# Kernel tuning notes

Measured on AMD Instinct MI355X. Metric: run time of the kernel, lower is better.

The kernel has to match this reference:

```python
import jax, jax.numpy as jnp
from jax import lax
import numpy as np

T, D, H, E, K = 4096, 1024, 2048, 8, 2

def setup_inputs() -> dict:
    key = jax.random.key(0)
    ks = jax.random.split(key, 5)
    x = jax.random.normal(ks[0], (T, D), dtype=jnp.float32)
    weights = jax.random.uniform(ks[1], (T, K), dtype=jnp.float32)
    indices = jax.random.randint(ks[2], (T, K), 0, E, dtype=jnp.int64)
    # GatedMLP params (bias=False): fc1 weight [2H, D], fc2 weight [D, H], stacked over experts
    W1 = jax.random.normal(ks[3], (E, 2 * H, D), dtype=jnp.float32) * 0.02
    W2 = jax.random.normal(ks[4], (E, D, H), dtype=jnp.float32) * 0.02
    return {"x": x, "weights": weights, "indices": indices, "W1": W1, "W2": W2}

def reference(x, weights, indices, W1, W2):
    # Combine per-token routing weights into a per-(token, expert) weight matrix.
    # Tokens not routed to expert e get weight 0, so the dense per-expert GatedMLP
    # weighted-sum is mathematically identical to the gather->MLP->scatter-add loop.
    onehot = jax.nn.one_hot(indices, E, dtype=weights.dtype)        # [T, K, E]
    w_te = jnp.einsum('tke,tk->et', onehot, weights)                # [E, T]

    def body(y, carry):
        W1e, W2e, we = carry                                        # [2H,D], [D,H], [T]
        h = x @ W1e.T                                               # [T, 2H]
        u, gate = jnp.split(h, 2, axis=-1)                          # [T, H] each
        out = (u * jax.nn.silu(gate)) @ W2e.T                       # [T, D]
        return y + out * we[:, None], None

    y, _ = lax.scan(body, jnp.zeros_like(x), (W1, W2, w_te))
    return y
```

## Files before the change

### kernel.cpp

```cpp
#include <hip/hip_runtime.h>
#include <stdint.h>

#define T_TOK 4096
#define D_DIM 1024
#define H_DIM 2048
#define E_EXP 8
#define K_TOP 2
#define NTK   (T_TOK * K_TOP)
#define MTILE 192
#define MAX_TILES 56

typedef short bf16x8 __attribute__((ext_vector_type(8)));
typedef float f32x4  __attribute__((ext_vector_type(4)));

#define MINI(a, b) ((a) < (b) ? (a) : (b))

__device__ __forceinline__ unsigned short f2bf(float f) {
  unsigned u = __float_as_uint(f);
  u += 0x7fffu + ((u >> 16) & 1u);
  return (unsigned short)(u >> 16);
}

#define GLDS16(gp, lp)                                                        \
  __builtin_amdgcn_global_load_lds(                                           \
      (const __attribute__((address_space(1))) void*)(gp),                    \
      (__attribute__((address_space(3))) void*)(lp), 16, 0, 0)



__global__ __launch_bounds__(256) void k_route_count(const int* __restrict__ idx,
                                                     int* __restrict__ meta) {
  __shared__ int h[E_EXP];
  int tid = threadIdx.x;
  if (tid < E_EXP) h[tid] = 0;
  __syncthreads();
  int i = blockIdx.x * 256 + tid;
  atomicAdd(&h[idx[i] & (E_EXP - 1)], 1);
  __syncthreads();
  if (tid < E_EXP) atomicAdd(&meta[tid], h[tid]);
}

__global__ __launch_bounds__(64) void k_route_plan(int* __restrict__ meta) {
  if (threadIdx.x) return;
  int off = 0, nt = 0;
  for (int e = 0; e < E_EXP; ++e) {
    int c = meta[e];
    meta[8 + e]  = off;
    meta[16 + e] = off;
    for (int r = 0; r < c; r += MTILE) {
      meta[32 + nt]  = e;
      meta[112 + nt] = off + r;
      meta[192 + nt] = MINI(MTILE, c - r);
      ++nt;
    }
    off += c;
  }
  meta[24] = nt;
}

__global__ __launch_bounds__(256) void k_route_scatter(const int* __restrict__ idx,
                                                       const float* __restrict__ w,
                                                       int* __restrict__ meta,
                                                       int* __restrict__ rows,
                                                       float* __restrict__ wv) {
  __shared__ int h[E_EXP], base[E_EXP];
  int tid = threadIdx.x;
  if (tid < E_EXP) h[tid] = 0;
  __syncthreads();
  int i = blockIdx.x * 256 + tid;
  int e = idx[i] & (E_EXP - 1);
  int r = atomicAdd(&h[e], 1);
  __syncthreads();
  if (tid < E_EXP) base[tid] = atomicAdd(&meta[16 + tid], h[tid]);
  __syncthreads();
  int p = base[e] + r;
  rows[p] = i >> 1;
  wv[p]   = w[i];
}

#define NX8   (T_TOK * D_DIM / 8)
#define NW18  (E_EXP * 2 * H_DIM * D_DIM / 8)
#define NW28  (E_EXP * D_DIM * H_DIM / 8)
#define NCVT8 (NX8 + NW18 + NW28)

__global__ __launch_bounds__(256) void k_cvt8(const float* __restrict__ x,
                                              const float* __restrict__ W1,
                                              const float* __restrict__ W2,
                                              unsigned short* __restrict__ xb,
                                              unsigned short* __restrict__ W1b,
                                              unsigned short* __restrict__ W2b) {
  long gid = (long)blockIdx.x * 256 + threadIdx.x;
  const float* src;
  unsigned short* dst;
  long i;
  if (gid < NX8) {
    src = x; dst = xb; i = gid;
  } else if (gid < NX8 + NW18) {
    src = W1; dst = W1b; i = gid - NX8;
  } else if (gid < NCVT8) {
    src = W2; dst = W2b; i = gid - (NX8 + NW18);
  } else return;
  float4 a = ((const float4*)src)[2 * i];
  float4 b = ((const float4*)src)[2 * i + 1];
  uint4 o;
  o.x = f2bf(a.x) | ((unsigned)f2bf(a.y) << 16);
  o.y = f2bf(a.z) | ((unsigned)f2bf(a.w) << 16);
  o.z = f2bf(b.x) | ((unsigned)f2bf(b.y) << 16);
  o.w = f2bf(b.z) | ((unsigned)f2bf(b.w) << 16);
  ((uint4*)dst)[i] = o;
}

__global__ __launch_bounds__(512, 2) void k_gemm1(
    const unsigned short* __restrict__ xb,
    const unsigned short* __restrict__ W1b,
    const int* __restrict__ meta,
    const int* __restrict__ rows,
    const float* __restrict__ wv,
    unsigned short* __restrict__ act) {
  int nt = meta[24];
  int tb = blockIdx.x;
  if (tb >= nt) return;
  int e     = meta[32 + tb];
  int r0    = meta[112 + tb];
  int valid = meta[192 + tb];
  int n0    = blockIdx.y * 128;

  __shared__ unsigned short lA[2][MTILE * 64];
  __shared__ unsigned short lB1[2][128 * 64];
  __shared__ unsigned short lB2[2][128 * 64];

  int tid  = threadIdx.x;
  int wave = tid >> 6, lane = tid & 63;
  int wm = wave >> 2, wn = wave & 3;

  const unsigned short* w1e = W1b + (size_t)e * (4096 * 1024);

  const unsigned short *pA[3], *pB1[2], *pB2[2];
#pragma unroll
  for (int it = 0; it < 3; ++it) {
    int c = it * 512 + tid;
    int r = c >> 3, cc = c & 7;
    int g = cc ^ (r & 7);
    int tok = rows[r0 + MINI(r, valid - 1)];
    pA[it] = xb + (size_t)tok * 1024 + g * 8;
  }
#pragma unroll
  for (int it = 0; it < 2; ++it) {
    int c = it * 512 + tid;
    int r = c >> 3, cc = c & 7;
    int g = cc ^ (r & 7);
    pB1[it] = w1e + (size_t)(n0 + r) * 1024 + g * 8;
    pB2[it] = w1e + (size_t)(2048 + n0 + r) * 1024 + g * 8;
  }

  auto STAGE = [&](int t, int b) {
    int k0 = t * 64;
#pragma unroll
    for (int it = 0; it < 3; ++it)
      GLDS16(pA[it] + k0, &lA[b][(it * 512 + wave * 64) * 8]);
#pragma unroll
    for (int it = 0; it < 2; ++it) {
      int lb = (it * 512 + wave * 64) * 8;
      GLDS16(pB1[it] + k0, &lB1[b][lb]);
      GLDS16(pB2[it] + k0, &lB2[b][lb]);
    }
  };

  f32x4 zero = {0.f, 0.f, 0.f, 0.f};
  f32x4 au[6][2], ag[6][2];
#pragma unroll
  for (int i = 0; i < 6; ++i)
#pragma unroll
    for (int j = 0; j < 2; ++j) { au[i][j] = zero; ag[i][j] = zero; }

  int fr = lane & 15, q = lane >> 4;

  STAGE(0, 0);
  for (int t = 0; t < 16; ++t) {
    int cb = t & 1;
    if (t < 15) {
      STAGE(t + 1, cb ^ 1);
      asm volatile("s_waitcnt vmcnt(7)" ::: "memory");
    } else {
      asm volatile("s_waitcnt vmcnt(0)" ::: "memory");
    }
    __builtin_amdgcn_s_barrier();
    __builtin_amdgcn_sched_barrier(0);
#pragma unroll
    for (int kk = 0; kk < 2; ++kk) {
      int co = (((kk << 2) + q) ^ (fr & 7)) * 8 + fr * 64;
      bf16x8 a[6];
#pragma unroll
      for (int i = 0; i < 6; ++i)
        a[i] = *(const bf16x8*)&lA[cb][(wm * 96 + i * 16) * 64 + co];
#pragma unroll
      for (int j = 0; j < 2; ++j) {
        bf16x8 bu = *(const bf16x8*)&lB1[cb][(wn * 32 + j * 16) * 64 + co];
        bf16x8 bg = *(const bf16x8*)&lB2[cb][(wn * 32 + j * 16) * 64 + co];
#pragma unroll
        for (int i = 0; i < 6; ++i) {
          au[i][j] = __builtin_amdgcn_mfma_f32_16x16x32_bf16(a[i], bu, au[i][j], 0, 0, 0);
          ag[i][j] = __builtin_amdgcn_mfma_f32_16x16x32_bf16(a[i], bg, ag[i][j], 0, 0, 0);
        }
      }
    }
    __builtin_amdgcn_s_barrier();
    __builtin_amdgcn_sched_barrier(0);
  }

#pragma unroll
  for (int i = 0; i < 6; ++i) {
#pragma unroll
    for (int reg = 0; reg < 4; ++reg) {
      int lm = wm * 96 + i * 16 + q * 4 + reg;
      if (lm < valid) {
        float wrow = wv[r0 + lm];
        size_t orow = (size_t)(r0 + lm) * 2048;
#pragma unroll
        for (int j = 0; j < 2; ++j) {
          float u = au[i][j][reg];
          float g = ag[i][j][reg];
          float s = g / (1.f + __expf(-g));
          act[orow + (n0 + wn * 32 + j * 16 + fr)] = f2bf(u * s * wrow);
        }
      }
    }
  }
}

__global__ __launch_bounds__(256, 2) void k_gemm2(
    const unsigned short* __restrict__ act,
    const unsigned short* __restrict__ W2b,
    const int* __restrict__ meta,
    const int* __restrict__ rows,
    float* __restrict__ out) {
  int nt = meta[24];
  int tb = blockIdx.x;
  if (tb >= nt) return;
  int e     = meta[32 + tb];
  int r0    = meta[112 + tb];
  int valid = meta[192 + tb];
  int n0    = blockIdx.y * 128;

  __shared__ unsigned short lA[2][MTILE * 64];
  __shared__ unsigned short lB[2][128 * 64];

  int tid  = threadIdx.x;
  int wave = tid >> 6, lane = tid & 63;
  int wm = wave >> 1, wn = wave & 1;

  const unsigned short* w2e = W2b + (size_t)e * (1024 * 2048);

  const unsigned short *pA[6], *pB[4];
#pragma unroll
  for (int it = 0; it < 6; ++it) {
    int c = it * 256 + tid;
    int r = c >> 3, cc = c & 7;
    int g = cc ^ (r & 7);
    pA[it] = act + (size_t)(r0 + MINI(r, valid - 1)) * 2048 + g * 8;
  }
#pragma unroll
  for (int it = 0; it < 4; ++it) {
    int c = it * 256 + tid;
    int r = c >> 3, cc = c & 7;
    int g = cc ^ (r & 7);
    pB[it] = w2e + (size_t)(n0 + r) * 2048 + g * 8;
  }

  auto STAGE = [&](int t, int b) {
    int k0 = t * 64;
#pragma unroll
    for (int it = 0; it < 6; ++it)
      GLDS16(pA[it] + k0, &lA[b][(it * 256 + wave * 64) * 8]);
#pragma unroll
    for (int it = 0; it < 4; ++it)
      GLDS16(pB[it] + k0, &lB[b][(it * 256 + wave * 64) * 8]);
  };

  f32x4 zero = {0.f, 0.f, 0.f, 0.f};
  f32x4 acc[6][4];
#pragma unroll
  for (int i = 0; i < 6; ++i)
#pragma unroll
    for (int j = 0; j < 4; ++j) acc[i][j] = zero;

  int fr = lane & 15, q = lane >> 4;

  STAGE(0, 0);
  for (int t = 0; t < 32; ++t) {
    int cb = t & 1;
    if (t < 31) {
      STAGE(t + 1, cb ^ 1);
      asm volatile("s_waitcnt vmcnt(10)" ::: "memory");
    } else {
      asm volatile("s_waitcnt vmcnt(0)" ::: "memory");
    }
    __builtin_amdgcn_s_barrier();
    __builtin_amdgcn_sched_barrier(0);
#pragma unroll
    for (int kk = 0; kk < 2; ++kk) {
      int co = (((kk << 2) + q) ^ (fr & 7)) * 8 + fr * 64;
      bf16x8 a[6];
#pragma unroll
      for (int i = 0; i < 6; ++i)
        a[i] = *(const bf16x8*)&lA[cb][(wm * 96 + i * 16) * 64 + co];
#pragma unroll
      for (int j = 0; j < 4; ++j) {
        bf16x8 b = *(const bf16x8*)&lB[cb][(wn * 64 + j * 16) * 64 + co];
#pragma unroll
        for (int i = 0; i < 6; ++i)
          acc[i][j] = __builtin_amdgcn_mfma_f32_16x16x32_bf16(a[i], b, acc[i][j], 0, 0, 0);
      }
    }
    __builtin_amdgcn_s_barrier();
    __builtin_amdgcn_sched_barrier(0);
  }

#pragma unroll
  for (int i = 0; i < 6; ++i) {
#pragma unroll
    for (int reg = 0; reg < 4; ++reg) {
      int lm = wm * 96 + i * 16 + q * 4 + reg;
      if (lm < valid) {
        int tok = rows[r0 + lm];
        float* op = out + (size_t)tok * 1024;
#pragma unroll
        for (int j = 0; j < 4; ++j)
          atomicAdd(&op[n0 + wn * 64 + j * 16 + fr], acc[i][j][reg]);
      }
    }
  }
}

extern "C" void kernel_launch(void* const* d_in, const int* in_sizes, int n_in,
                              void* d_out, int out_size, void* d_ws, size_t ws_size,
                              hipStream_t stream) {
  const float* x  = (const float*)d_in[0];
  const float* w  = (const float*)d_in[1];
  const int*  idx = (const int*)d_in[2];
  const float* W1 = (const float*)d_in[3];
  const float* W2 = (const float*)d_in[4];
  float* out = (float*)d_out;

  char* ws = (char*)d_ws;
  unsigned short* W1b = (unsigned short*)(ws);
  unsigned short* W2b = (unsigned short*)(ws + 67108864);
  unsigned short* xb  = (unsigned short*)(ws + 100663296);
  unsigned short* act = (unsigned short*)(ws + 109051904);
  int*   rows = (int*)(ws + 142606336);
  float* wv   = (float*)(ws + 142639104);
  int*   meta = (int*)(ws + 142671872);

  hipMemsetAsync(d_out, 0, (size_t)out_size * sizeof(float), stream);
  hipMemsetAsync(meta, 0, 1088, stream);

  k_cvt8<<<(NCVT8 + 255) / 256, 256, 0, stream>>>(x, W1, W2, xb, W1b, W2b);
  k_route_count<<<32, 256, 0, stream>>>(idx, meta);
  k_route_plan<<<1, 64, 0, stream>>>(meta);
  k_route_scatter<<<32, 256, 0, stream>>>(idx, w, meta, rows, wv);

  dim3 g1(MAX_TILES, H_DIM / 128);
  dim3 g2(MAX_TILES, D_DIM / 128);
  k_gemm1<<<g1, 512, 0, stream>>>(xb, W1b, meta, rows, wv, act);
  k_gemm2<<<g2, 256, 0, stream>>>(act, W2b, meta, rows, out);
}
```

Before: 462.1 us.

## Restructure MoE GEMMs with separate tile sizes, 4-stage pipeline, and XCD-aware block mapping

Both grouped GEMM kernels are rewritten. gemm1 now uses 256-row tiles and gemm2 uses 128-row tiles, with a separate routing plan for each. The loads become a 4-slot ring buffer with K-step 32, loads for future stages issue between two MFMA half-phases under setprio, and the LDS swizzle is new. A 1-D grid remaps block IDs so that blocks sharing an expert tile land on the same XCD, aiming for better L2 reuse and deeper latency hiding. This adds more barriers per step and finer-grained waits, and the wave mapping changes occupancy.

After: 495.1 us. 1.07x slower.

```diff
diff --git a/kernel.cpp b/kernel.cpp
--- a/kernel.cpp
+++ b/kernel.cpp
@@ -7,13 +7,16 @@
 #define E_EXP 8
 #define K_TOP 2
 #define NTK   (T_TOK * K_TOP)
-#define MTILE 192
-#define MAX_TILES 56
+#define MT1 256
+#define MT2 128
+#define MAXT1 48
+#define MAXT2 72
 
 typedef short bf16x8 __attribute__((ext_vector_type(8)));
 typedef float f32x4  __attribute__((ext_vector_type(4)));
 
 #define MINI(a, b) ((a) < (b) ? (a) : (b))
+#define MFMA_BF16 __builtin_amdgcn_mfma_f32_16x16x32_bf16
 
 __device__ __forceinline__ unsigned short f2bf(float f) {
   unsigned u = __float_as_uint(f);
@@ -25,7 +28,6 @@
   __builtin_amdgcn_global_load_lds(                                           \
       (const __attribute__((address_space(1))) void*)(gp),                    \
       (__attribute__((address_space(3))) void*)(lp), 16, 0, 0)
-
 
 
 __global__ __launch_bounds__(256) void k_route_count(const int* __restrict__ idx,
@@ -42,20 +44,27 @@
 
 __global__ __launch_bounds__(64) void k_route_plan(int* __restrict__ meta) {
   if (threadIdx.x) return;
-  int off = 0, nt = 0;
+  int off = 0, nt1 = 0, nt2 = 0;
   for (int e = 0; e < E_EXP; ++e) {
     int c = meta[e];
     meta[8 + e]  = off;
     meta[16 + e] = off;
-    for (int r = 0; r < c; r += MTILE) {
-      meta[32 + nt]  = e;
-      meta[112 + nt] = off + r;
-      meta[192 + nt] = MINI(MTILE, c - r);
-      ++nt;
+    for (int r = 0; r < c; r += MT1) {
+      meta[32 + nt1]  = e;
+      meta[80 + nt1]  = off + r;
+      meta[128 + nt1] = MINI(MT1, c - r);
+      ++nt1;
+    }
+    for (int r = 0; r < c; r += MT2) {
+      meta[176 + nt2] = e;
+      meta[248 + nt2] = off + r;
+      meta[320 + nt2] = MINI(MT2, c - r);
+      ++nt2;
     }
     off += c;
   }
-  meta[24] = nt;
+  meta[24] = nt1;
+  meta[25] = nt2;
 }
 
 __global__ __launch_bounds__(256) void k_route_scatter(const int* __restrict__ idx,
@@ -117,111 +126,156 @@
     const int* __restrict__ rows,
     const float* __restrict__ wv,
     unsigned short* __restrict__ act) {
+  int bid = blockIdx.x;
   int nt = meta[24];
-  int tb = blockIdx.x;
+  int xcd = bid & 7, jj = bid >> 3;
+  int y   = jj & 15;
+  int tb  = ((jj >> 4) << 3) + xcd;
   if (tb >= nt) return;
   int e     = meta[32 + tb];
-  int r0    = meta[112 + tb];
-  int valid = meta[192 + tb];
-  int n0    = blockIdx.y * 128;
-
-  __shared__ unsigned short lA[2][MTILE * 64];
-  __shared__ unsigned short lB1[2][128 * 64];
-  __shared__ unsigned short lB2[2][128 * 64];
+  int r0    = meta[80 + tb];
+  int valid = meta[128 + tb];
+  int n0    = y << 7;
+
+  __shared__ unsigned short lA[4][8192];
+  __shared__ unsigned short lB[4][8192];
 
   int tid  = threadIdx.x;
   int wave = tid >> 6, lane = tid & 63;
   int wm = wave >> 2, wn = wave & 3;
+  int fr = lane & 15, q = lane >> 4;
+  int swz8 = (q ^ ((fr >> 1) & 3)) << 3;
 
   const unsigned short* w1e = W1b + (size_t)e * (4096 * 1024);
 
-  const unsigned short *pA[3], *pB1[2], *pB2[2];
-#pragma unroll
-  for (int it = 0; it < 3; ++it) {
-    int c = it * 512 + tid;
-    int r = c >> 3, cc = c & 7;
-    int g = cc ^ (r & 7);
+  const unsigned short *pA[2], *pB[2];
+#pragma unroll
+  for (int it = 0; it < 2; ++it) {
+    int s = it * 512 + tid;
+    int r = s >> 2;
+    int c = (s & 3) ^ ((s >> 3) & 3);
     int tok = rows[r0 + MINI(r, valid - 1)];
-    pA[it] = xb + (size_t)tok * 1024 + g * 8;
-  }
-#pragma unroll
-  for (int it = 0; it < 2; ++it) {
-    int c = it * 512 + tid;
-    int r = c >> 3, cc = c & 7;
-    int g = cc ^ (r & 7);
-    pB1[it] = w1e + (size_t)(n0 + r) * 1024 + g * 8;
-    pB2[it] = w1e + (size_t)(2048 + n0 + r) * 1024 + g * 8;
-  }
-
-  auto STAGE = [&](int t, int b) {
-    int k0 = t * 64;
-#pragma unroll
-    for (int it = 0; it < 3; ++it)
-      GLDS16(pA[it] + k0, &lA[b][(it * 512 + wave * 64) * 8]);
-#pragma unroll
-    for (int it = 0; it < 2; ++it) {
-      int lb = (it * 512 + wave * 64) * 8;
-      GLDS16(pB1[it] + k0, &lB1[b][lb]);
-      GLDS16(pB2[it] + k0, &lB2[b][lb]);
-    }
+    pA[it] = xb + (size_t)tok * 1024 + c * 8;
+    int wrow = (r < 128) ? (n0 + r) : (1920 + n0 + r);
+    pB[it] = w1e + (size_t)wrow * 1024 + c * 8;
+  }
+
+  auto ISSUE_A = [&](int g) {
+    int sl = g & 3, ko = g * 32;
+#pragma unroll
+    for (int it = 0; it < 2; ++it)
+      GLDS16(pA[it] + ko, &lA[sl][(it * 512 + wave * 64) * 8]);
   };
+  auto ISSUE_B = [&](int g) {
+    int sl = g & 3, ko = g * 32;
+#pragma unroll
+    for (int it = 0; it < 2; ++it)
+      GLDS16(pB[it] + ko, &lB[sl][(it * 512 + wave * 64) * 8]);
+  };
 
   f32x4 zero = {0.f, 0.f, 0.f, 0.f};
-  f32x4 au[6][2], ag[6][2];
-#pragma unroll
-  for (int i = 0; i < 6; ++i)
-#pragma unroll
-    for (int j = 0; j < 2; ++j) { au[i][j] = zero; ag[i][j] = zero; }
-
-  int fr = lane & 15, q = lane >> 4;
-
-  STAGE(0, 0);
-  for (int t = 0; t < 16; ++t) {
-    int cb = t & 1;
-    if (t < 15) {
-      STAGE(t + 1, cb ^ 1);
-      asm volatile("s_waitcnt vmcnt(7)" ::: "memory");
-    } else {
-      asm volatile("s_waitcnt vmcnt(0)" ::: "memory");
-    }
-    __builtin_amdgcn_s_barrier();
-    __builtin_amdgcn_sched_barrier(0);
-#pragma unroll
-    for (int kk = 0; kk < 2; ++kk) {
-      int co = (((kk << 2) + q) ^ (fr & 7)) * 8 + fr * 64;
-      bf16x8 a[6];
-#pragma unroll
-      for (int i = 0; i < 6; ++i)
-        a[i] = *(const bf16x8*)&lA[cb][(wm * 96 + i * 16) * 64 + co];
-#pragma unroll
-      for (int j = 0; j < 2; ++j) {
-        bf16x8 bu = *(const bf16x8*)&lB1[cb][(wn * 32 + j * 16) * 64 + co];
-        bf16x8 bg = *(const bf16x8*)&lB2[cb][(wn * 32 + j * 16) * 64 + co];
-#pragma unroll
-        for (int i = 0; i < 6; ++i) {
-          au[i][j] = __builtin_amdgcn_mfma_f32_16x16x32_bf16(a[i], bu, au[i][j], 0, 0, 0);
-          ag[i][j] = __builtin_amdgcn_mfma_f32_16x16x32_bf16(a[i], bg, ag[i][j], 0, 0, 0);
-        }
-      }
-    }
-    __builtin_amdgcn_s_barrier();
-    __builtin_amdgcn_sched_barrier(0);
-  }
-
-#pragma unroll
-  for (int i = 0; i < 6; ++i) {
+  f32x4 au[8][2], ag[8][2];
+#pragma unroll
+  for (int i = 0; i < 8; ++i)
+#pragma unroll
+    for (int n = 0; n < 2; ++n) { au[i][n] = zero; ag[i][n] = zero; }
+
+  int abase = ((wm << 7) + fr) * 32 + swz8;
+  int ubase = ((wn << 5) + fr) * 32 + swz8;
+
+  ISSUE_A(0); ISSUE_B(0);
+  ISSUE_A(1); ISSUE_B(1);
+  ISSUE_A(2); ISSUE_B(2);
+  asm volatile("s_waitcnt vmcnt(8)" ::: "memory");
+  __builtin_amdgcn_s_barrier();
+
+  for (int g = 0; g < 32; ++g) {
+    int sl = g & 3;
+    const unsigned short* A = lA[sl];
+    const unsigned short* B = lB[sl];
+
+    bf16x8 a0 = *(const bf16x8*)&A[abase + 0 * 512];
+    bf16x8 a1 = *(const bf16x8*)&A[abase + 1 * 512];
+    bf16x8 a2 = *(const bf16x8*)&A[abase + 2 * 512];
+    bf16x8 a3 = *(const bf16x8*)&A[abase + 3 * 512];
+    bf16x8 bu0 = *(const bf16x8*)&B[ubase];
+    bf16x8 bu1 = *(const bf16x8*)&B[ubase + 512];
+    bf16x8 bg0 = *(const bf16x8*)&B[ubase + 4096];
+    bf16x8 bg1 = *(const bf16x8*)&B[ubase + 4608];
+    if (g < 29) ISSUE_A(g + 3);
+    __builtin_amdgcn_sched_barrier(0);
+    __builtin_amdgcn_s_barrier();
+    asm volatile("s_waitcnt lgkmcnt(0)" ::: "memory");
+    __builtin_amdgcn_sched_barrier(0);
+    __builtin_amdgcn_s_setprio(1);
+    au[0][0] = MFMA_BF16(a0, bu0, au[0][0], 0, 0, 0);
+    au[0][1] = MFMA_BF16(a0, bu1, au[0][1], 0, 0, 0);
+    ag[0][0] = MFMA_BF16(a0, bg0, ag[0][0], 0, 0, 0);
+    ag[0][1] = MFMA_BF16(a0, bg1, ag[0][1], 0, 0, 0);
+    au[1][0] = MFMA_BF16(a1, bu0, au[1][0], 0, 0, 0);
+    au[1][1] = MFMA_BF16(a1, bu1, au[1][1], 0, 0, 0);
+    ag[1][0] = MFMA_BF16(a1, bg0, ag[1][0], 0, 0, 0);
+    ag[1][1] = MFMA_BF16(a1, bg1, ag[1][1], 0, 0, 0);
+    au[2][0] = MFMA_BF16(a2, bu0, au[2][0], 0, 0, 0);
+    au[2][1] = MFMA_BF16(a2, bu1, au[2][1], 0, 0, 0);
+    ag[2][0] = MFMA_BF16(a2, bg0, ag[2][0], 0, 0, 0);
+    ag[2][1] = MFMA_BF16(a2, bg1, ag[2][1], 0, 0, 0);
+    au[3][0] = MFMA_BF16(a3, bu0, au[3][0], 0, 0, 0);
+    au[3][1] = MFMA_BF16(a3, bu1, au[3][1], 0, 0, 0);
+    ag[3][0] = MFMA_BF16(a3, bg0, ag[3][0], 0, 0, 0);
+    ag[3][1] = MFMA_BF16(a3, bg1, ag[3][1], 0, 0, 0);
+    __builtin_amdgcn_s_setprio(0);
+    __builtin_amdgcn_sched_barrier(0);
+    __builtin_amdgcn_s_barrier();
+
+    bf16x8 a4 = *(const bf16x8*)&A[abase + 2048 + 0 * 512];
+    bf16x8 a5 = *(const bf16x8*)&A[abase + 2048 + 1 * 512];
+    bf16x8 a6 = *(const bf16x8*)&A[abase + 2048 + 2 * 512];
+    bf16x8 a7 = *(const bf16x8*)&A[abase + 2048 + 3 * 512];
+    if (g < 29) ISSUE_B(g + 3);
+    if (g < 29)      asm volatile("s_waitcnt vmcnt(8)" ::: "memory");
+    else if (g == 29) asm volatile("s_waitcnt vmcnt(4)" ::: "memory");
+    else if (g == 30) asm volatile("s_waitcnt vmcnt(0)" ::: "memory");
+    __builtin_amdgcn_sched_barrier(0);
+    __builtin_amdgcn_s_barrier();
+    asm volatile("s_waitcnt lgkmcnt(0)" ::: "memory");
+    __builtin_amdgcn_sched_barrier(0);
+    __builtin_amdgcn_s_setprio(1);
+    au[4][0] = MFMA_BF16(a4, bu0, au[4][0], 0, 0, 0);
+    au[4][1] = MFMA_BF16(a4, bu1, au[4][1], 0, 0, 0);
+    ag[4][0] = MFMA_BF16(a4, bg0, ag[4][0], 0, 0, 0);
+    ag[4][1] = MFMA_BF16(a4, bg1, ag[4][1], 0, 0, 0);
+    au[5][0] = MFMA_BF16(a5, bu0, au[5][0], 0, 0, 0);
+    au[5][1] = MFMA_BF16(a5, bu1, au[5][1], 0, 0, 0);
+    ag[5][0] = MFMA_BF16(a5, bg0, ag[5][0], 0, 0, 0);
+    ag[5][1] = MFMA_BF16(a5, bg1, ag[5][1], 0, 0, 0);
+    au[6][0] = MFMA_BF16(a6, bu0, au[6][0], 0, 0, 0);
+    au[6][1] = MFMA_BF16(a6, bu1, au[6][1], 0, 0, 0);
+    ag[6][0] = MFMA_BF16(a6, bg0, ag[6][0], 0, 0, 0);
+    ag[6][1] = MFMA_BF16(a6, bg1, ag[6][1], 0, 0, 0);
+    au[7][0] = MFMA_BF16(a7, bu0, au[7][0], 0, 0, 0);
+    au[7][1] = MFMA_BF16(a7, bu1, au[7][1], 0, 0, 0);
+    ag[7][0] = MFMA_BF16(a7, bg0, ag[7][0], 0, 0, 0);
+    ag[7][1] = MFMA_BF16(a7, bg1, ag[7][1], 0, 0, 0);
+    __builtin_amdgcn_s_setprio(0);
+    __builtin_amdgcn_sched_barrier(0);
+    __builtin_amdgcn_s_barrier();
+  }
+
+#pragma unroll
+  for (int mi = 0; mi < 8; ++mi) {
 #pragma unroll
     for (int reg = 0; reg < 4; ++reg) {
-      int lm = wm * 96 + i * 16 + q * 4 + reg;
+      int lm = (wm << 7) + mi * 16 + q * 4 + reg;
       if (lm < valid) {
         float wrow = wv[r0 + lm];
-        size_t orow = (size_t)(r0 + lm) * 2048;
-#pragma unroll
-        for (int j = 0; j < 2; ++j) {
-          float u = au[i][j][reg];
-          float g = ag[i][j][reg];
-          float s = g / (1.f + __expf(-g));
-          act[orow + (n0 + wn * 32 + j * 16 + fr)] = f2bf(u * s * wrow);
+        size_t orow = (size_t)(r0 + lm) * 2048 + n0 + (wn << 5);
+#pragma unroll
+        for (int n = 0; n < 2; ++n) {
+          float u = au[mi][n][reg];
+          float gg = ag[mi][n][reg];
+          float s = gg / (1.f + __expf(-gg));
+          act[orow + n * 16 + fr] = f2bf(u * s * wrow);
         }
       }
     }
@@ -234,99 +288,121 @@
     const int* __restrict__ meta,
     const int* __restrict__ rows,
     float* __restrict__ out) {
-  int nt = meta[24];
-  int tb = blockIdx.x;
+  int bid = blockIdx.x;
+  int nt = meta[25];
+  int xcd = bid & 7, jj = bid >> 3;
+  int y   = jj & 7;
+  int tb  = ((jj >> 3) << 3) + xcd;
   if (tb >= nt) return;
-  int e     = meta[32 + tb];
-  int r0    = meta[112 + tb];
-  int valid = meta[192 + tb];
-  int n0    = blockIdx.y * 128;
-
-  __shared__ unsigned short lA[2][MTILE * 64];
-  __shared__ unsigned short lB[2][128 * 64];
+  int e     = meta[176 + tb];
+  int r0    = meta[248 + tb];
+  int valid = meta[320 + tb];
+  int n0    = y << 7;
+
+  __shared__ unsigned short lA[4][4096];
+  __shared__ unsigned short lB[4][4096];
 
   int tid  = threadIdx.x;
   int wave = tid >> 6, lane = tid & 63;
   int wm = wave >> 1, wn = wave & 1;
+  int fr = lane & 15, q = lane >> 4;
+  int swz8 = (q ^ ((fr >> 1) & 3)) << 3;
 
   const unsigned short* w2e = W2b + (size_t)e * (1024 * 2048);
 
-  const unsigned short *pA[6], *pB[4];
-#pragma unroll
-  for (int it = 0; it < 6; ++it) {
-    int c = it * 256 + tid;
-    int r = c >> 3, cc = c & 7;
-    int g = cc ^ (r & 7);
-    pA[it] = act + (size_t)(r0 + MINI(r, valid - 1)) * 2048 + g * 8;
-  }
-#pragma unroll
-  for (int it = 0; it < 4; ++it) {
-    int c = it * 256 + tid;
-    int r = c >> 3, cc = c & 7;
-    int g = cc ^ (r & 7);
-    pB[it] = w2e + (size_t)(n0 + r) * 2048 + g * 8;
-  }
-
-  auto STAGE = [&](int t, int b) {
-    int k0 = t * 64;
-#pragma unroll
-    for (int it = 0; it < 6; ++it)
-      GLDS16(pA[it] + k0, &lA[b][(it * 256 + wave * 64) * 8]);
-#pragma unroll
-    for (int it = 0; it < 4; ++it)
-      GLDS16(pB[it] + k0, &lB[b][(it * 256 + wave * 64) * 8]);
+  const unsigned short *pA[2], *pB[2];
+#pragma unroll
+  for (int it = 0; it < 2; ++it) {
+    int s = it * 256 + tid;
+    int r = s >> 2;
+    int c = (s & 3) ^ ((s >> 3) & 3);
+    pA[it] = act + (size_t)(r0 + MINI(r, valid - 1)) * 2048 + c * 8;
+    pB[it] = w2e + (size_t)(n0 + r) * 2048 + c * 8;
+  }
+
+  auto ISSUE_A = [&](int g) {
+    int sl = g & 3, ko = g * 32;
+#pragma unroll
+    for (int it = 0; it < 2; ++it)
+      GLDS16(pA[it] + ko, &lA[sl][(it * 256 + wave * 64) * 8]);
   };
+  auto ISSUE_B = [&](int g) {
+    int sl = g & 3, ko = g * 32;
+#pragma unroll
+    for (int it = 0; it < 2; ++it)
+      GLDS16(pB[it] + ko, &lB[sl][(it * 256 + wave * 64) * 8]);
+  };
 
   f32x4 zero = {0.f, 0.f, 0.f, 0.f};
-  f32x4 acc[6][4];
-#pragma unroll
-  for (int i = 0; i < 6; ++i)
-#pragma unroll
-    for (int j = 0; j < 4; ++j) acc[i][j] = zero;
-
-  int fr = lane & 15, q = lane >> 4;
-
-  STAGE(0, 0);
-  for (int t = 0; t < 32; ++t) {
-    int cb = t & 1;
-    if (t < 31) {
-      STAGE(t + 1, cb ^ 1);
-      asm volatile("s_waitcnt vmcnt(10)" ::: "memory");
-    } else {
-      asm volatile("s_waitcnt vmcnt(0)" ::: "memory");
-    }
-    __builtin_amdgcn_s_barrier();
-    __builtin_amdgcn_sched_barrier(0);
-#pragma unroll
-    for (int kk = 0; kk < 2; ++kk) {
-      int co = (((kk << 2) + q) ^ (fr & 7)) * 8 + fr * 64;
-      bf16x8 a[6];
-#pragma unroll
-      for (int i = 0; i < 6; ++i)
-        a[i] = *(const bf16x8*)&lA[cb][(wm * 96 + i * 16) * 64 + co];
-#pragma unroll
-      for (int j = 0; j < 4; ++j) {
-        bf16x8 b = *(const bf16x8*)&lB[cb][(wn * 64 + j * 16) * 64 + co];
-#pragma unroll
-        for (int i = 0; i < 6; ++i)
-          acc[i][j] = __builtin_amdgcn_mfma_f32_16x16x32_bf16(a[i], b, acc[i][j], 0, 0, 0);
-      }
-    }
-    __builtin_amdgcn_s_barrier();
-    __builtin_amdgcn_sched_barrier(0);
-  }
-
-#pragma unroll
-  for (int i = 0; i < 6; ++i) {
+  f32x4 acc[4][4];
+#pragma unroll
+  for (int i = 0; i < 4; ++i)
+#pragma unroll
+    for (int n = 0; n < 4; ++n) acc[i][n] = zero;
+
+  int abase = ((wm << 6) + fr) * 32 + swz8;
+  int bbase = ((wn << 6) + fr) * 32 + swz8;
+
+  ISSUE_A(0); ISSUE_B(0);
+  ISSUE_A(1); ISSUE_B(1);
+  ISSUE_A(2); ISSUE_B(2);
+  asm volatile("s_waitcnt vmcnt(8)" ::: "memory");
+  __builtin_amdgcn_s_barrier();
+
+  for (int g = 0; g < 64; ++g) {
+    int sl = g & 3;
+    const unsigned short* A = lA[sl];
+    const unsigned short* B = lB[sl];
+
+    bf16x8 a0 = *(const bf16x8*)&A[abase + 0 * 512];
+    bf16x8 a1 = *(const bf16x8*)&A[abase + 1 * 512];
+    bf16x8 a2 = *(const bf16x8*)&A[abase + 2 * 512];
+    bf16x8 a3 = *(const bf16x8*)&A[abase + 3 * 512];
+    bf16x8 b0 = *(const bf16x8*)&B[bbase + 0 * 512];
+    bf16x8 b1 = *(const bf16x8*)&B[bbase + 1 * 512];
+    bf16x8 b2 = *(const bf16x8*)&B[bbase + 2 * 512];
+    bf16x8 b3 = *(const bf16x8*)&B[bbase + 3 * 512];
+    if (g < 61) { ISSUE_A(g + 3); ISSUE_B(g + 3); }
+    if (g < 61)      asm volatile("s_waitcnt vmcnt(8)" ::: "memory");
+    else if (g == 61) asm volatile("s_waitcnt vmcnt(4)" ::: "memory");
+    else if (g == 62) asm volatile("s_waitcnt vmcnt(0)" ::: "memory");
+    __builtin_amdgcn_sched_barrier(0);
+    __builtin_amdgcn_s_barrier();
+    asm volatile("s_waitcnt lgkmcnt(0)" ::: "memory");
+    __builtin_amdgcn_sched_barrier(0);
+    __builtin_amdgcn_s_setprio(1);
+    acc[0][0] = MFMA_BF16(a0, b0, acc[0][0], 0, 0, 0);
+    acc[0][1] = MFMA_BF16(a0, b1, acc[0][1], 0, 0, 0);
+    acc[0][2] = MFMA_BF16(a0, b2, acc[0][2], 0, 0, 0);
+    acc[0][3] = MFMA_BF16(a0, b3, acc[0][3], 0, 0, 0);
+    acc[1][0] = MFMA_BF16(a1, b0, acc[1][0], 0, 0, 0);
+    acc[1][1] = MFMA_BF16(a1, b1, acc[1][1], 0, 0, 0);
+    acc[1][2] = MFMA_BF16(a1, b2, acc[1][2], 0, 0, 0);
+    acc[1][3] = MFMA_BF16(a1, b3, acc[1][3], 0, 0, 0);
+    acc[2][0] = MFMA_BF16(a2, b0, acc[2][0], 0, 0, 0);
+    acc[2][1] = MFMA_BF16(a2, b1, acc[2][1], 0, 0, 0);
+    acc[2][2] = MFMA_BF16(a2, b2, acc[2][2], 0, 0, 0);
+    acc[2][3] = MFMA_BF16(a2, b3, acc[2][3], 0, 0, 0);
+    acc[3][0] = MFMA_BF16(a3, b0, acc[3][0], 0, 0, 0);
+    acc[3][1] = MFMA_BF16(a3, b1, acc[3][1], 0, 0, 0);
+    acc[3][2] = MFMA_BF16(a3, b2, acc[3][2], 0, 0, 0);
+    acc[3][3] = MFMA_BF16(a3, b3, acc[3][3], 0, 0, 0);
+    __builtin_amdgcn_s_setprio(0);
+    __builtin_amdgcn_sched_barrier(0);
+    __builtin_amdgcn_s_barrier();
+  }
+
+#pragma unroll
+  for (int i = 0; i < 4; ++i) {
 #pragma unroll
     for (int reg = 0; reg < 4; ++reg) {
-      int lm = wm * 96 + i * 16 + q * 4 + reg;
+      int lm = (wm << 6) + i * 16 + q * 4 + reg;
       if (lm < valid) {
         int tok = rows[r0 + lm];
-        float* op = out + (size_t)tok * 1024;
-#pragma unroll
-        for (int j = 0; j < 4; ++j)
-          atomicAdd(&op[n0 + wn * 64 + j * 16 + fr], acc[i][j][reg]);
+        float* op = out + (size_t)tok * 1024 + n0 + (wn << 6);
+#pragma unroll
+        for (int n = 0; n < 4; ++n)
+          atomicAdd(&op[n * 16 + fr], acc[i][n][reg]);
       }
     }
   }
@@ -352,15 +428,13 @@
   int*   meta = (int*)(ws + 142671872);
 
   hipMemsetAsync(d_out, 0, (size_t)out_size * sizeof(float), stream);
-  hipMemsetAsync(meta, 0, 1088, stream);
+  hipMemsetAsync(meta, 0, 2048, stream);
 
   k_cvt8<<<(NCVT8 + 255) / 256, 256, 0, stream>>>(x, W1, W2, xb, W1b, W2b);
   k_route_count<<<32, 256, 0, stream>>>(idx, meta);
   k_route_plan<<<1, 64, 0, stream>>>(meta);
   k_route_scatter<<<32, 256, 0, stream>>>(idx, w, meta, rows, wv);
 
-  dim3 g1(MAX_TILES, H_DIM / 128);
-  dim3 g2(MAX_TILES, D_DIM / 128);
-  k_gemm1<<<g1, 512, 0, stream>>>(xb, W1b, meta, rows, wv, act);
-  k_gemm2<<<g2, 256, 0, stream>>>(act, W2b, meta, rows, out);
-}
+  k_gemm1<<<MAXT1 * 16, 512, 0, stream>>>(xb, W1b, meta, rows, wv, act);
+  k_gemm2<<<MAXT2 * 8, 256, 0, stream>>>(act, W2b, meta, rows, out);
+}
```
